# Optimization experiments

Measured on AMD Instinct MI355X. Metric: run time of the kernel, lower is better.

## Reference

```python
import jax, jax.numpy as jnp
import numpy as np

FILTER_SIZE = 1
SPATIAL_SCALE = 1.0 / 16.0  # 1 / feature_stride


def _g(u):
    # Antiderivative of the triangular bilinear kernel max(0, 1-|t|),
    # evaluated as cumulative integral from -inf to u.
    u = jnp.clip(u, -1.0, 1.0)
    return jnp.where(u < 0.0, 0.5 * (u + 1.0) ** 2, 1.0 - 0.5 * (1.0 - u) ** 2)


def _interval_weights(a, b, size):
    # a, b: (N, fs) bin start/end in feature-grid coords.
    # Returns (N, fs, size): integral of the triangle kernel centered at each
    # pixel index over [a, b] (pixels outside the grid contribute zero, matching
    # PrRoIPool's zero-padded reads).
    idx = jnp.arange(size, dtype=a.dtype)
    return _g(b[..., None] - idx) - _g(a[..., None] - idx)


def setup_inputs() -> dict:
    key = jax.random.key(0)
    k1, k2 = jax.random.split(key)
    feat = jax.random.normal(k1, (128, 256, 36, 36), dtype=jnp.float32)
    r = jax.random.uniform(k2, (128, 4), dtype=jnp.float32)
    # (x, y, w, h) in image coords for a 576x576 image
    bb = jnp.stack([r[:, 0] * 400.0, r[:, 1] * 400.0,
                    16.0 + r[:, 2] * 144.0, 16.0 + r[:, 3] * 144.0], axis=1)
    return {"feat": feat, "bb": bb}


def reference(feat, bb):
    # FilterPool.forward: bbox (x,y,w,h) -> (x0,y0,x1,y1), then PrRoIPool2D
    # with pooled size FILTER_SIZE x FILTER_SIZE and spatial_scale 1/16.
    N, C, H, W = feat.shape
    bb = bb.reshape(-1, 4)
    fs = FILTER_SIZE
    x0 = bb[:, 0] * SPATIAL_SCALE
    y0 = bb[:, 1] * SPATIAL_SCALE
    x1 = (bb[:, 0] + bb[:, 2]) * SPATIAL_SCALE
    y1 = (bb[:, 1] + bb[:, 3]) * SPATIAL_SCALE
    bin_w = (x1 - x0) / fs  # (N,)
    bin_h = (y1 - y0) / fs
    j = jnp.arange(fs, dtype=feat.dtype)
    bx0 = x0[:, None] + j * bin_w[:, None]  # (N, fs)
    bx1 = bx0 + bin_w[:, None]
    by0 = y0[:, None] + j * bin_h[:, None]
    by1 = by0 + bin_h[:, None]
    wx = _interval_weights(bx0, bx1, W)  # (N, fs, W)
    wy = _interval_weights(by0, by1, H)  # (N, fs, H)
    # Integral of bilinear interpolation over each bin = separable contraction.
    pooled = jnp.einsum('nchw,nph,nqw->ncpq', feat, wy, wx)
    area = (jnp.maximum(bin_w, 0.0) * jnp.maximum(bin_h, 0.0))[:, None, None, None]
    return jnp.where(area > 0.0, pooled / jnp.maximum(area, 1e-30), 0.0)
```

## Files before the change

kernel.cpp:

```cpp
#include <hip/hip_runtime.h>

#define NC 256
#define FH 36
#define FW 36
#define SCALE (1.0f/16.0f)

__device__ __forceinline__ float g_fn(float u) {
    u = fminf(1.0f, fmaxf(-1.0f, u));
    if (u < 0.0f) { float t = u + 1.0f; return 0.5f * t * t; }
    else          { float t = 1.0f - u; return 1.0f - 0.5f * t * t; }
}

__global__ __launch_bounds__(256) void filterpool_kernel(
    const float* __restrict__ feat,
    const float* __restrict__ bb,
    float* __restrict__ out)
{
    const int n    = blockIdx.x;
    const int cg   = blockIdx.y;
    const int t    = threadIdx.x;
    const int lane = t & 63;
    const int wave = t >> 6;
    const int c    = cg * 4 + wave;

    __shared__ float wx[FW];
    __shared__ float wy[FH];

    const float bx = bb[n*4+0], by = bb[n*4+1];
    const float bw = bb[n*4+2], bh = bb[n*4+3];
    const float x0 = bx * SCALE,        y0 = by * SCALE;
    const float x1 = (bx + bw) * SCALE, y1 = (by + bh) * SCALE;

    if (t < FW) {
        float fw = (float)t;
        wx[t] = g_fn(x1 - fw) - g_fn(x0 - fw);
    } else if (t < FW + FH) {
        int h = t - FW;
        float fh = (float)h;
        wy[h] = g_fn(y1 - fh) - g_fn(y0 - fh);
    }
    __syncthreads();

    const float4* fptr = (const float4*)(feat + ((size_t)n * NC + c) * (FH * FW));
    float acc = 0.0f;
    #pragma unroll 2
    for (int q = lane; q < (FH * FW) / 4; q += 64) {
        float4 v = fptr[q];
        int h  = q / 9;
        int w0 = (q - h * 9) * 4;
        float wyh = wy[h];
        acc += wyh * (v.x * wx[w0]     + v.y * wx[w0 + 1]
                    + v.z * wx[w0 + 2] + v.w * wx[w0 + 3]);
    }

    #pragma unroll
    for (int off = 32; off > 0; off >>= 1)
        acc += __shfl_down(acc, off, 64);

    if (lane == 0) {
        float bin_w = x1 - x0, bin_h = y1 - y0;
        float area = fmaxf(bin_w, 0.0f) * fmaxf(bin_h, 0.0f);
        float res  = (area > 0.0f) ? (acc / fmaxf(area, 1e-30f)) : 0.0f;
        out[(size_t)n * NC + c] = res;
    }
}

extern "C" void kernel_launch(void* const* d_in, const int* in_sizes, int n_in,
                              void* d_out, int out_size, void* d_ws, size_t ws_size,
                              hipStream_t stream) {
    const float* feat = (const float*)d_in[0];
    const float* bb   = (const float*)d_in[1];
    float* out        = (float*)d_out;
    dim3 grid(128, 64);
    filterpool_kernel<<<grid, 256, 0, stream>>>(feat, bb, out);
}
```

Baseline: 234.7 us.

## Process four channels per wave with fully unrolled loads and fewer blocks

Each wave now reduces four channels at once, reusing the per-position x/y weights and issuing four independent float4 loads per iteration. The loop is fully unrolled with an explicit tail, and the grid shrinks to 16 channels per block, amortizing the weight setup and barrier. The goal is more memory-level parallelism on a bandwidth-bound streaming reduction, at the cost of higher register use and fewer blocks.

```diff
diff --git a/kernel.cpp b/kernel.cpp
--- a/kernel.cpp
+++ b/kernel.cpp
@@ -3,7 +3,10 @@
 #define NC 256
 #define FH 36
 #define FW 36
+#define Q4 ((FH*FW)/4)
 #define SCALE (1.0f/16.0f)
+#define CPW 4
+#define CPB 16
 
 __device__ __forceinline__ float g_fn(float u) {
     u = fminf(1.0f, fmaxf(-1.0f, u));
@@ -16,12 +19,12 @@
     const float* __restrict__ bb,
     float* __restrict__ out)
 {
-    const int n    = blockIdx.x;
-    const int cg   = blockIdx.y;
+    const int cg   = blockIdx.x;
+    const int n    = blockIdx.y;
     const int t    = threadIdx.x;
     const int lane = t & 63;
     const int wave = t >> 6;
-    const int c    = cg * 4 + wave;
+    const int c0   = cg * CPB + wave * CPW;
 
     __shared__ float wx[FW];
     __shared__ float wy[FH];
@@ -32,36 +35,62 @@
     const float x1 = (bx + bw) * SCALE, y1 = (by + bh) * SCALE;
 
     if (t < FW) {
-        float fw = (float)t;
-        wx[t] = g_fn(x1 - fw) - g_fn(x0 - fw);
+        wx[t] = g_fn(x1 - (float)t) - g_fn(x0 - (float)t);
     } else if (t < FW + FH) {
         int h = t - FW;
-        float fh = (float)h;
-        wy[h] = g_fn(y1 - fh) - g_fn(y0 - fh);
+        wy[h] = g_fn(y1 - (float)h) - g_fn(y0 - (float)h);
     }
     __syncthreads();
 
-    const float4* fptr = (const float4*)(feat + ((size_t)n * NC + c) * (FH * FW));
-    float acc = 0.0f;
-    #pragma unroll 2
-    for (int q = lane; q < (FH * FW) / 4; q += 64) {
-        float4 v = fptr[q];
+    const float4* f0 = (const float4*)(feat + ((size_t)n * NC + c0) * (FH * FW));
+    float acc0 = 0.f, acc1 = 0.f, acc2 = 0.f, acc3 = 0.f;
+
+    #pragma unroll
+    for (int it = 0; it < 5; ++it) {
+        int q  = lane + it * 64;
         int h  = q / 9;
         int w0 = (q - h * 9) * 4;
         float wyh = wy[h];
-        acc += wyh * (v.x * wx[w0]     + v.y * wx[w0 + 1]
-                    + v.z * wx[w0 + 2] + v.w * wx[w0 + 3]);
+        float wa = wx[w0], wb = wx[w0+1], wc = wx[w0+2], wd = wx[w0+3];
+        float4 v0 = f0[q];
+        float4 v1 = f0[Q4   + q];
+        float4 v2 = f0[2*Q4 + q];
+        float4 v3 = f0[3*Q4 + q];
+        acc0 += wyh * (v0.x*wa + v0.y*wb + v0.z*wc + v0.w*wd);
+        acc1 += wyh * (v1.x*wa + v1.y*wb + v1.z*wc + v1.w*wd);
+        acc2 += wyh * (v2.x*wa + v2.y*wb + v2.z*wc + v2.w*wd);
+        acc3 += wyh * (v3.x*wa + v3.y*wb + v3.z*wc + v3.w*wd);
+    }
+    if (lane < 4) {
+        int q  = 320 + lane;
+        int h  = q / 9;
+        int w0 = (q - h * 9) * 4;
+        float wyh = wy[h];
+        float wa = wx[w0], wb = wx[w0+1], wc = wx[w0+2], wd = wx[w0+3];
+        float4 v0 = f0[q];
+        float4 v1 = f0[Q4   + q];
+        float4 v2 = f0[2*Q4 + q];
+        float4 v3 = f0[3*Q4 + q];
+        acc0 += wyh * (v0.x*wa + v0.y*wb + v0.z*wc + v0.w*wd);
+        acc1 += wyh * (v1.x*wa + v1.y*wb + v1.z*wc + v1.w*wd);
+        acc2 += wyh * (v2.x*wa + v2.y*wb + v2.z*wc + v2.w*wd);
+        acc3 += wyh * (v3.x*wa + v3.y*wb + v3.z*wc + v3.w*wd);
     }
 
     #pragma unroll
-    for (int off = 32; off > 0; off >>= 1)
-        acc += __shfl_down(acc, off, 64);
+    for (int off = 32; off > 0; off >>= 1) {
+        acc0 += __shfl_xor(acc0, off, 64);
+        acc1 += __shfl_xor(acc1, off, 64);
+        acc2 += __shfl_xor(acc2, off, 64);
+        acc3 += __shfl_xor(acc3, off, 64);
+    }
 
     if (lane == 0) {
         float bin_w = x1 - x0, bin_h = y1 - y0;
         float area = fmaxf(bin_w, 0.0f) * fmaxf(bin_h, 0.0f);
-        float res  = (area > 0.0f) ? (acc / fmaxf(area, 1e-30f)) : 0.0f;
-        out[(size_t)n * NC + c] = res;
+        float inv  = (area > 0.0f) ? (1.0f / fmaxf(area, 1e-30f)) : 0.0f;
+        float4 r = make_float4(acc0 * inv, acc1 * inv, acc2 * inv, acc3 * inv);
+        *(float4*)(out + (size_t)n * NC + c0) = r;
     }
 }
 
@@ -71,6 +100,6 @@
     const float* feat = (const float*)d_in[0];
     const float* bb   = (const float*)d_in[1];
     float* out        = (float*)d_out;
-    dim3 grid(128, 64);
+    dim3 grid(NC / CPB, 128);
     filterpool_kernel<<<grid, 256, 0, stream>>>(feat, bb, out);
 }
```

After: 235.2 us. No clear change (+0.2%).
